# Kernel tuning notes

Measured on AMD Instinct MI355X. Metric: run time of the kernel, lower is better.

Reference implementation:

```python
import jax, jax.numpy as jnp
import numpy as np

TOP_K = 8


def setup_inputs() -> dict:
    key = jax.random.key(0)
    k1, k2, k3, k4, k5 = jax.random.split(key, 5)
    B, S, H, E, I = 1, 2048, 2048, 32, 768
    return {
        "hidden_states": jax.random.normal(k1, (B, S, H), dtype=jnp.float32),
        "gate_w": jax.random.normal(k2, (E, H), dtype=jnp.float32) * (H ** -0.5),
        "w_gate_proj": jax.random.normal(k3, (E, I, H), dtype=jnp.float32) * (H ** -0.5),
        "w_up_proj": jax.random.normal(k4, (E, I, H), dtype=jnp.float32) * (H ** -0.5),
        "w_down_proj": jax.random.normal(k5, (E, H, I), dtype=jnp.float32) * (I ** -0.5),
    }


def _masked_routing(router_logits):
    # norm_topk_prob=True branch: topk logits -> softmax over the k selected
    T, E = router_logits.shape
    sel_w, sel_e = jax.lax.top_k(router_logits, TOP_K)          # [T,k]
    sel_w = jax.nn.softmax(sel_w.astype(jnp.float32), axis=1)    # [T,k]
    rows = jnp.arange(T)[:, None]
    masked = jnp.zeros((T, E), dtype=jnp.float32).at[rows, sel_e].set(sel_w)
    count = jnp.zeros((E,), dtype=jnp.int32).at[sel_e.reshape(-1)].add(1)
    return masked, count


def reference(hidden_states, gate_w, w_gate_proj, w_up_proj, w_down_proj):
    B, S, H = hidden_states.shape
    x = hidden_states.reshape(-1, H)                              # [T,H]
    router_logits = x @ gate_w.T                                  # [T,E]
    masked_w, _count = _masked_routing(router_logits)
    # custom_moe_glu: per-expert GLU MLP, combined with masked routing weights
    g = jnp.einsum("th,eih->tei", x, w_gate_proj)                # [T,E,I]
    u = jnp.einsum("th,eih->tei", x, w_up_proj)                  # [T,E,I]
    h = jax.nn.silu(g) * u                                        # [T,E,I]
    h = h * masked_w[:, :, None]                                  # zero unselected experts
    out = jnp.einsum("tei,ehi->th", h, w_down_proj)              # [T,H]
    return out.reshape(B, S, H)
```

## Files before the change

kernel.cpp:

```cpp
#include <hip/hip_runtime.h>

#define T_TOK 2048
#define H_DIM 2048
#define E_NUM 32
#define I_DIM 768
#define TOPK 8

typedef __attribute__((ext_vector_type(8))) _Float16 f16x8;
typedef __attribute__((ext_vector_type(4))) _Float16 f16x4;
typedef __attribute__((ext_vector_type(4))) float f32x4;

__global__ __launch_bounds__(256) void cvt_x_kernel(const float* __restrict__ x,
                                                    _Float16* __restrict__ xh) {
    int i = blockIdx.x * 256 + threadIdx.x;
    f32x4 f = ((const f32x4*)x)[i];
    f16x4 h;
    h[0] = (_Float16)f[0]; h[1] = (_Float16)f[1];
    h[2] = (_Float16)f[2]; h[3] = (_Float16)f[3];
    ((f16x4*)xh)[i] = h;
}

__global__ __launch_bounds__(256) void router_kernel(const float* __restrict__ x,
                                                     const float* __restrict__ gw,
                                                     int* __restrict__ sel_e,
                                                     float* __restrict__ sel_w,
                                                     int* __restrict__ counts) {
    int t = blockIdx.x;
    int tid = threadIdx.x, lane = tid & 63, wave = tid >> 6;
    __shared__ float logits[E_NUM];
    const float* xr = x + (size_t)t * H_DIM;
    float xv[32];
#pragma unroll
    for (int c = 0; c < 32; ++c) xv[c] = xr[lane + c * 64];
    for (int j = 0; j < 8; ++j) {
        int e = wave * 8 + j;
        const float* wr = gw + (size_t)e * H_DIM;
        float acc = 0.f;
#pragma unroll
        for (int c = 0; c < 32; ++c) acc += xv[c] * wr[lane + c * 64];
#pragma unroll
        for (int s = 32; s > 0; s >>= 1) acc += __shfl_xor(acc, s, 64);
        if (lane == 0) logits[e] = acc;
    }
    __syncthreads();
    if (tid == 0) {
        float lg[E_NUM];
        for (int e2 = 0; e2 < E_NUM; ++e2) lg[e2] = logits[e2];
        unsigned taken = 0;
        float sv[TOPK]; int se[TOPK];
        for (int k = 0; k < TOPK; ++k) {
            float best = -3.4e38f; int bi = 0;
            for (int e2 = 0; e2 < E_NUM; ++e2)
                if (!((taken >> e2) & 1u) && lg[e2] > best) { best = lg[e2]; bi = e2; }
            taken |= 1u << bi; sv[k] = best; se[k] = bi;
        }
        float m = sv[0], s = 0.f;
        for (int k = 0; k < TOPK; ++k) { sv[k] = expf(sv[k] - m); s += sv[k]; }
        float inv = 1.f / s;
        for (int k = 0; k < TOPK; ++k) {
            sel_e[t * TOPK + k] = se[k];
            sel_w[t * TOPK + k] = sv[k] * inv;
            atomicAdd(&counts[se[k]], 1);
        }
    }
}

__global__ void scan_kernel(const int* __restrict__ counts, int* __restrict__ offs) {
    if (threadIdx.x == 0) {
        int s = 0;
        for (int e = 0; e < E_NUM; ++e) { offs[e] = s; s += counts[e]; }
        offs[E_NUM] = s;
    }
}

__global__ __launch_bounds__(256) void scatter_kernel(const int* __restrict__ sel_e,
                                                      const float* __restrict__ sel_w,
                                                      const int* __restrict__ offs,
                                                      int* __restrict__ cursor,
                                                      int* __restrict__ pair_token,
                                                      float* __restrict__ pair_w) {
    int t = blockIdx.x * 256 + threadIdx.x;
    if (t >= T_TOK) return;
    for (int k = 0; k < TOPK; ++k) {
        int e = sel_e[t * TOPK + k];
        int pos = atomicAdd(&cursor[e], 1);
        int slot = offs[e] + pos;
        pair_token[slot] = t;
        pair_w[slot] = sel_w[t * TOPK + k];
    }
}

__global__ __launch_bounds__(256, 2) void mlp1_kernel(const _Float16* __restrict__ xh,
                                                      const float* __restrict__ wg,
                                                      const float* __restrict__ wu,
                                                      const int* __restrict__ offs,
                                                      const int* __restrict__ pair_token,
                                                      const float* __restrict__ pair_w,
                                                      _Float16* __restrict__ h_buf) {
    int e = blockIdx.z, mt = blockIdx.y, nt = blockIdx.x;
    int base = offs[e], cnt = offs[e + 1] - base;
    if (mt * 128 >= cnt) return;
    int tid = threadIdx.x, lane = tid & 63, wave = tid >> 6;

    __shared__ _Float16 As[128 * 40];
    __shared__ _Float16 Bg[128 * 40];
    __shared__ _Float16 Bu[128 * 40];

    const _Float16* aSrc[2]; int aDst[2];
#pragma unroll
    for (int i = 0; i < 2; ++i) {
        int c = tid + i * 256;
        int row = c >> 2, col8 = c & 3;
        int g = mt * 128 + row;
        int tok = (g < cnt) ? pair_token[base + g] : pair_token[base];
        aSrc[i] = xh + (size_t)tok * H_DIM + col8 * 8;
        aDst[i] = row * 40 + col8 * 8;
    }
    const float* gSrc[4]; const float* uSrc[4]; int bDst[4];
#pragma unroll
    for (int i = 0; i < 4; ++i) {
        int c = tid + i * 256;
        int row = c >> 3, col4 = c & 7;
        size_t wOff = ((size_t)e * I_DIM + nt * 128 + row) * H_DIM + col4 * 4;
        gSrc[i] = wg + wOff; uSrc[i] = wu + wOff;
        bDst[i] = row * 40 + col4 * 4;
    }

    const f32x4 zero = {0.f, 0.f, 0.f, 0.f};
    f32x4 accg[4][4], accu[4][4];
#pragma unroll
    for (int mi = 0; mi < 4; ++mi)
#pragma unroll
        for (int ni = 0; ni < 4; ++ni) { accg[mi][ni] = zero; accu[mi][ni] = zero; }

    int m16 = lane & 15, quad = lane >> 4, wm = wave >> 1, wn = wave & 1;

    for (int k0 = 0; k0 < H_DIM; k0 += 32) {
#pragma unroll
        for (int i = 0; i < 2; ++i)
            *(f16x8*)&As[aDst[i]] = *(const f16x8*)(aSrc[i] + k0);
#pragma unroll
        for (int i = 0; i < 4; ++i) {
            f32x4 fg = *(const f32x4*)(gSrc[i] + k0);
            f32x4 fu = *(const f32x4*)(uSrc[i] + k0);
            f16x4 hg, hu;
#pragma unroll
            for (int q = 0; q < 4; ++q) { hg[q] = (_Float16)fg[q]; hu[q] = (_Float16)fu[q]; }
            *(f16x4*)&Bg[bDst[i]] = hg;
            *(f16x4*)&Bu[bDst[i]] = hu;
        }
        __syncthreads();
        f16x8 a[4], bg[4], bu[4];
#pragma unroll
        for (int mi = 0; mi < 4; ++mi)
            a[mi] = *(const f16x8*)&As[(wm * 64 + mi * 16 + m16) * 40 + quad * 8];
#pragma unroll
        for (int ni = 0; ni < 4; ++ni) {
            int r = (wn * 64 + ni * 16 + m16) * 40 + quad * 8;
            bg[ni] = *(const f16x8*)&Bg[r];
            bu[ni] = *(const f16x8*)&Bu[r];
        }
#pragma unroll
        for (int mi = 0; mi < 4; ++mi)
#pragma unroll
            for (int ni = 0; ni < 4; ++ni) {
                accg[mi][ni] = __builtin_amdgcn_mfma_f32_16x16x32_f16(a[mi], bg[ni], accg[mi][ni], 0, 0, 0);
                accu[mi][ni] = __builtin_amdgcn_mfma_f32_16x16x32_f16(a[mi], bu[ni], accu[mi][ni], 0, 0, 0);
            }
        __syncthreads();
    }

#pragma unroll
    for (int mi = 0; mi < 4; ++mi) {
#pragma unroll
        for (int reg = 0; reg < 4; ++reg) {
            int rloc = wm * 64 + mi * 16 + quad * 4 + reg;
            int g = mt * 128 + rloc;
            if (g >= cnt) continue;
            int slot = base + g;
            float pw = pair_w[slot];
#pragma unroll
            for (int ni = 0; ni < 4; ++ni) {
                int col = nt * 128 + wn * 64 + ni * 16 + m16;
                float gv = accg[mi][ni][reg];
                float uv = accu[mi][ni][reg];
                float hv = (gv / (1.f + expf(-gv))) * uv * pw;
                h_buf[(size_t)slot * I_DIM + col] = (_Float16)hv;
            }
        }
    }
}

__global__ __launch_bounds__(256, 2) void mlp2_kernel(const _Float16* __restrict__ h_buf,
                                                      const float* __restrict__ wd,
                                                      const int* __restrict__ offs,
                                                      const int* __restrict__ pair_token,
                                                      float* __restrict__ out) {
    int e = blockIdx.z, mt = blockIdx.y, nt = blockIdx.x;
    int base = offs[e], cnt = offs[e + 1] - base;
    if (mt * 128 >= cnt) return;
    int tid = threadIdx.x, lane = tid & 63, wave = tid >> 6;

    __shared__ _Float16 As[128 * 40];
    __shared__ _Float16 Bs[128 * 40];

    const _Float16* aSrc[2]; int aDst[2];
#pragma unroll
    for (int i = 0; i < 2; ++i) {
        int c = tid + i * 256;
        int row = c >> 2, col8 = c & 3;
        int g = mt * 128 + row;
        int slot = (g < cnt) ? (base + g) : base;
        aSrc[i] = h_buf + (size_t)slot * I_DIM + col8 * 8;
        aDst[i] = row * 40 + col8 * 8;
    }
    const float* bSrc[4]; int bDst[4];
#pragma unroll
    for (int i = 0; i < 4; ++i) {
        int c = tid + i * 256;
        int row = c >> 3, col4 = c & 7;
        bSrc[i] = wd + ((size_t)e * H_DIM + nt * 128 + row) * I_DIM + col4 * 4;
        bDst[i] = row * 40 + col4 * 4;
    }

    const f32x4 zero = {0.f, 0.f, 0.f, 0.f};
    f32x4 acc[4][4];
#pragma unroll
    for (int mi = 0; mi < 4; ++mi)
#pragma unroll
        for (int ni = 0; ni < 4; ++ni) acc[mi][ni] = zero;

    int m16 = lane & 15, quad = lane >> 4, wm = wave >> 1, wn = wave & 1;

    for (int k0 = 0; k0 < I_DIM; k0 += 32) {
#pragma unroll
        for (int i = 0; i < 2; ++i)
            *(f16x8*)&As[aDst[i]] = *(const f16x8*)(aSrc[i] + k0);
#pragma unroll
        for (int i = 0; i < 4; ++i) {
            f32x4 f = *(const f32x4*)(bSrc[i] + k0);
            f16x4 h;
#pragma unroll
            for (int q = 0; q < 4; ++q) h[q] = (_Float16)f[q];
            *(f16x4*)&Bs[bDst[i]] = h;
        }
        __syncthreads();
        f16x8 a[4], b[4];
#pragma unroll
        for (int mi = 0; mi < 4; ++mi)
            a[mi] = *(const f16x8*)&As[(wm * 64 + mi * 16 + m16) * 40 + quad * 8];
#pragma unroll
        for (int ni = 0; ni < 4; ++ni)
            b[ni] = *(const f16x8*)&Bs[(wn * 64 + ni * 16 + m16) * 40 + quad * 8];
#pragma unroll
        for (int mi = 0; mi < 4; ++mi)
#pragma unroll
            for (int ni = 0; ni < 4; ++ni)
                acc[mi][ni] = __builtin_amdgcn_mfma_f32_16x16x32_f16(a[mi], b[ni], acc[mi][ni], 0, 0, 0);
        __syncthreads();
    }

#pragma unroll
    for (int mi = 0; mi < 4; ++mi) {
#pragma unroll
        for (int reg = 0; reg < 4; ++reg) {
            int rloc = wm * 64 + mi * 16 + quad * 4 + reg;
            int g = mt * 128 + rloc;
            if (g >= cnt) continue;
            int t = pair_token[base + g];
#pragma unroll
            for (int ni = 0; ni < 4; ++ni) {
                int col = nt * 128 + wn * 64 + ni * 16 + m16;
                atomicAdd(&out[(size_t)t * H_DIM + col], acc[mi][ni][reg]);
            }
        }
    }
}

extern "C" void kernel_launch(void* const* d_in, const int* in_sizes, int n_in,
                              void* d_out, int out_size, void* d_ws, size_t ws_size,
                              hipStream_t stream) {
    const float* x  = (const float*)d_in[0];
    const float* gw = (const float*)d_in[1];
    const float* wg = (const float*)d_in[2];
    const float* wu = (const float*)d_in[3];
    const float* wd = (const float*)d_in[4];
    float* out = (float*)d_out;

    char* ws = (char*)d_ws;
    int*      sel_e      = (int*)(ws + 0);
    float*    sel_w      = (float*)(ws + 65536);
    int*      counts     = (int*)(ws + 131072);
    int*      cursor     = (int*)(ws + 131200);
    int*      offs       = (int*)(ws + 131328);
    int*      pair_token = (int*)(ws + 131584);
    float*    pair_w     = (float*)(ws + 197120);
    _Float16* xh         = (_Float16*)(ws + 262656);
    _Float16* h_buf      = (_Float16*)(ws + 8651264);

    hipMemsetAsync(ws + 131072, 0, 256, stream);
    hipMemsetAsync(d_out, 0, (size_t)T_TOK * H_DIM * sizeof(float), stream);

    cvt_x_kernel<<<(T_TOK * H_DIM / 4) / 256, 256, 0, stream>>>(x, xh);
    router_kernel<<<T_TOK, 256, 0, stream>>>(x, gw, sel_e, sel_w, counts);
    scan_kernel<<<1, 64, 0, stream>>>(counts, offs);
    scatter_kernel<<<T_TOK / 256, 256, 0, stream>>>(sel_e, sel_w, offs, cursor, pair_token, pair_w);
    mlp1_kernel<<<dim3(6, 16, 32), 256, 0, stream>>>(xh, wg, wu, offs, pair_token, pair_w, h_buf);
    mlp2_kernel<<<dim3(16, 16, 32), 256, 0, stream>>>(h_buf, wd, offs, pair_token, out);
}
```

Before: 954.0 us.

## Reshape MoE GEMM tiles to 256x64 and parallelize router top-k with wave shuffles

Changes both expert GEMM kernels from 128x128 tiles to 256-row by 64-column tiles, with each wave owning 64 rows. Fewer fp32 weight elements are loaded and converted per tile, so weight traffic per output is meant to drop as token rows increase. Grid order is swapped so row tiles vary fastest, which may improve L2 reuse of weight tiles across blocks. The router's serial single-thread top-k becomes a wave-wide shuffle argmax, with the tradeoff that experts averaging ~512 tokens leave partially empty 256-row tiles.

```diff
diff --git a/kernel.cpp b/kernel.cpp
--- a/kernel.cpp
+++ b/kernel.cpp
@@ -43,24 +43,33 @@
         if (lane == 0) logits[e] = acc;
     }
     __syncthreads();
-    if (tid == 0) {
-        float lg[E_NUM];
-        for (int e2 = 0; e2 < E_NUM; ++e2) lg[e2] = logits[e2];
-        unsigned taken = 0;
+    if (wave == 0) {
+        float v = (lane < E_NUM) ? logits[lane] : -3.4e38f;
+        int idx = lane;
         float sv[TOPK]; int se[TOPK];
+#pragma unroll
         for (int k = 0; k < TOPK; ++k) {
-            float best = -3.4e38f; int bi = 0;
-            for (int e2 = 0; e2 < E_NUM; ++e2)
-                if (!((taken >> e2) & 1u) && lg[e2] > best) { best = lg[e2]; bi = e2; }
-            taken |= 1u << bi; sv[k] = best; se[k] = bi;
-        }
-        float m = sv[0], s = 0.f;
-        for (int k = 0; k < TOPK; ++k) { sv[k] = expf(sv[k] - m); s += sv[k]; }
-        float inv = 1.f / s;
-        for (int k = 0; k < TOPK; ++k) {
-            sel_e[t * TOPK + k] = se[k];
-            sel_w[t * TOPK + k] = sv[k] * inv;
-            atomicAdd(&counts[se[k]], 1);
+            float bv = v; int bi = idx;
+#pragma unroll
+            for (int s = 32; s > 0; s >>= 1) {
+                float ov = __shfl_xor(bv, s, 64);
+                int oi = __shfl_xor(bi, s, 64);
+                if (ov > bv || (ov == bv && oi < bi)) { bv = ov; bi = oi; }
+            }
+            sv[k] = bv; se[k] = bi;
+            if (lane == bi) v = -3.4e38f;
+        }
+        if (lane == 0) {
+            float m = sv[0], s = 0.f;
+#pragma unroll
+            for (int k = 0; k < TOPK; ++k) { sv[k] = expf(sv[k] - m); s += sv[k]; }
+            float inv = 1.f / s;
+#pragma unroll
+            for (int k = 0; k < TOPK; ++k) {
+                sel_e[t * TOPK + k] = se[k];
+                sel_w[t * TOPK + k] = sv[k] * inv;
+                atomicAdd(&counts[se[k]], 1);
+            }
         }
     }
 }
@@ -97,31 +106,31 @@
                                                       const int* __restrict__ pair_token,
                                                       const float* __restrict__ pair_w,
                                                       _Float16* __restrict__ h_buf) {
-    int e = blockIdx.z, mt = blockIdx.y, nt = blockIdx.x;
+    int mt = blockIdx.x, nt = blockIdx.y, e = blockIdx.z;
     int base = offs[e], cnt = offs[e + 1] - base;
-    if (mt * 128 >= cnt) return;
+    if (mt * 256 >= cnt) return;
     int tid = threadIdx.x, lane = tid & 63, wave = tid >> 6;
 
-    __shared__ _Float16 As[128 * 40];
-    __shared__ _Float16 Bg[128 * 40];
-    __shared__ _Float16 Bu[128 * 40];
-
-    const _Float16* aSrc[2]; int aDst[2];
-#pragma unroll
-    for (int i = 0; i < 2; ++i) {
+    __shared__ _Float16 As[256 * 40];
+    __shared__ _Float16 Bg[64 * 40];
+    __shared__ _Float16 Bu[64 * 40];
+
+    const _Float16* aSrc[4]; int aDst[4];
+#pragma unroll
+    for (int i = 0; i < 4; ++i) {
         int c = tid + i * 256;
         int row = c >> 2, col8 = c & 3;
-        int g = mt * 128 + row;
+        int g = mt * 256 + row;
         int tok = (g < cnt) ? pair_token[base + g] : pair_token[base];
         aSrc[i] = xh + (size_t)tok * H_DIM + col8 * 8;
         aDst[i] = row * 40 + col8 * 8;
     }
-    const float* gSrc[4]; const float* uSrc[4]; int bDst[4];
-#pragma unroll
-    for (int i = 0; i < 4; ++i) {
+    const float* gSrc[2]; const float* uSrc[2]; int bDst[2];
+#pragma unroll
+    for (int i = 0; i < 2; ++i) {
         int c = tid + i * 256;
         int row = c >> 3, col4 = c & 7;
-        size_t wOff = ((size_t)e * I_DIM + nt * 128 + row) * H_DIM + col4 * 4;
+        size_t wOff = ((size_t)e * I_DIM + nt * 64 + row) * H_DIM + col4 * 4;
         gSrc[i] = wg + wOff; uSrc[i] = wu + wOff;
         bDst[i] = row * 40 + col4 * 4;
     }
@@ -133,14 +142,14 @@
 #pragma unroll
         for (int ni = 0; ni < 4; ++ni) { accg[mi][ni] = zero; accu[mi][ni] = zero; }
 
-    int m16 = lane & 15, quad = lane >> 4, wm = wave >> 1, wn = wave & 1;
+    int m16 = lane & 15, quad = lane >> 4, wm = wave;
 
     for (int k0 = 0; k0 < H_DIM; k0 += 32) {
 #pragma unroll
-        for (int i = 0; i < 2; ++i)
+        for (int i = 0; i < 4; ++i)
             *(f16x8*)&As[aDst[i]] = *(const f16x8*)(aSrc[i] + k0);
 #pragma unroll
-        for (int i = 0; i < 4; ++i) {
+        for (int i = 0; i < 2; ++i) {
             f32x4 fg = *(const f32x4*)(gSrc[i] + k0);
             f32x4 fu = *(const f32x4*)(uSrc[i] + k0);
             f16x4 hg, hu;
@@ -156,7 +165,7 @@
             a[mi] = *(const f16x8*)&As[(wm * 64 + mi * 16 + m16) * 40 + quad * 8];
 #pragma unroll
         for (int ni = 0; ni < 4; ++ni) {
-            int r = (wn * 64 + ni * 16 + m16) * 40 + quad * 8;
+            int r = (ni * 16 + m16) * 40 + quad * 8;
             bg[ni] = *(const f16x8*)&Bg[r];
             bu[ni] = *(const f16x8*)&Bu[r];
         }
@@ -175,13 +184,13 @@
 #pragma unroll
         for (int reg = 0; reg < 4; ++reg) {
             int rloc = wm * 64 + mi * 16 + quad * 4 + reg;
-            int g = mt * 128 + rloc;
+            int g = mt * 256 + rloc;
             if (g >= cnt) continue;
             int slot = base + g;
             float pw = pair_w[slot];
 #pragma unroll
             for (int ni = 0; ni < 4; ++ni) {
-                int col = nt * 128 + wn * 64 + ni * 16 + m16;
+                int col = nt * 64 + ni * 16 + m16;
                 float gv = accg[mi][ni][reg];
                 float uv = accu[mi][ni][reg];
                 float hv = (gv / (1.f + expf(-gv))) * uv * pw;
@@ -196,30 +205,30 @@
                                                       const int* __restrict__ offs,
                                                       const int* __restrict__ pair_token,
                                                       float* __restrict__ out) {
-    int e = blockIdx.z, mt = blockIdx.y, nt = blockIdx.x;
+    int mt = blockIdx.x, nt = blockIdx.y, e = blockIdx.z;
     int base = offs[e], cnt = offs[e + 1] - base;
-    if (mt * 128 >= cnt) return;
+    if (mt * 256 >= cnt) return;
     int tid = threadIdx.x, lane = tid & 63, wave = tid >> 6;
 
-    __shared__ _Float16 As[128 * 40];
-    __shared__ _Float16 Bs[128 * 40];
-
-    const _Float16* aSrc[2]; int aDst[2];
-#pragma unroll
-    for (int i = 0; i < 2; ++i) {
+    __shared__ _Float16 As[256 * 40];
+    __shared__ _Float16 Bs[64 * 40];
+
+    const _Float16* aSrc[4]; int aDst[4];
+#pragma unroll
+    for (int i = 0; i < 4; ++i) {
         int c = tid + i * 256;
         int row = c >> 2, col8 = c & 3;
-        int g = mt * 128 + row;
+        int g = mt * 256 + row;
         int slot = (g < cnt) ? (base + g) : base;
         aSrc[i] = h_buf + (size_t)slot * I_DIM + col8 * 8;
         aDst[i] = row * 40 + col8 * 8;
     }
-    const float* bSrc[4]; int bDst[4];
-#pragma unroll
-    for (int i = 0; i < 4; ++i) {
+    const float* bSrc[2]; int bDst[2];
+#pragma unroll
+    for (int i = 0; i < 2; ++i) {
         int c = tid + i * 256;
         int row = c >> 3, col4 = c & 7;
-        bSrc[i] = wd + ((size_t)e * H_DIM + nt * 128 + row) * I_DIM + col4 * 4;
+        bSrc[i] = wd + ((size_t)e * H_DIM + nt * 64 + row) * I_DIM + col4 * 4;
         bDst[i] = row * 40 + col4 * 4;
     }
 
@@ -230,14 +239,14 @@
 #pragma unroll
         for (int ni = 0; ni < 4; ++ni) acc[mi][ni] = zero;
 
-    int m16 = lane & 15, quad = lane >> 4, wm = wave >> 1, wn = wave & 1;
+    int m16 = lane & 15, quad = lane >> 4, wm = wave;
 
     for (int k0 = 0; k0 < I_DIM; k0 += 32) {
 #pragma unroll
-        for (int i = 0; i < 2; ++i)
+        for (int i = 0; i < 4; ++i)
             *(f16x8*)&As[aDst[i]] = *(const f16x8*)(aSrc[i] + k0);
 #pragma unroll
-        for (int i = 0; i < 4; ++i) {
+        for (int i = 0; i < 2; ++i) {
             f32x4 f = *(const f32x4*)(bSrc[i] + k0);
             f16x4 h;
 #pragma unroll
@@ -251,7 +260,7 @@
             a[mi] = *(const f16x8*)&As[(wm * 64 + mi * 16 + m16) * 40 + quad * 8];
 #pragma unroll
         for (int ni = 0; ni < 4; ++ni)
-            b[ni] = *(const f16x8*)&Bs[(wn * 64 + ni * 16 + m16) * 40 + quad * 8];
+            b[ni] = *(const f16x8*)&Bs[(ni * 16 + m16) * 40 + quad * 8];
 #pragma unroll
         for (int mi = 0; mi < 4; ++mi)
 #pragma unroll
@@ -265,12 +274,12 @@
 #pragma unroll
         for (int reg = 0; reg < 4; ++reg) {
             int rloc = wm * 64 + mi * 16 + quad * 4 + reg;
-            int g = mt * 128 + rloc;
+            int g = mt * 256 + rloc;
             if (g >= cnt) continue;
             int t = pair_token[base + g];
 #pragma unroll
             for (int ni = 0; ni < 4; ++ni) {
-                int col = nt * 128 + wn * 64 + ni * 16 + m16;
+                int col = nt * 64 + ni * 16 + m16;
                 atomicAdd(&out[(size_t)t * H_DIM + col], acc[mi][ni][reg]);
             }
         }
@@ -305,6 +314,6 @@
     router_kernel<<<T_TOK, 256, 0, stream>>>(x, gw, sel_e, sel_w, counts);
     scan_kernel<<<1, 64, 0, stream>>>(counts, offs);
     scatter_kernel<<<T_TOK / 256, 256, 0, stream>>>(sel_e, sel_w, offs, cursor, pair_token, pair_w);
-    mlp1_kernel<<<dim3(6, 16, 32), 256, 0, stream>>>(xh, wg, wu, offs, pair_token, pair_w, h_buf);
-    mlp2_kernel<<<dim3(16, 16, 32), 256, 0, stream>>>(h_buf, wd, offs, pair_token, out);
-}
+    mlp1_kernel<<<dim3(8, 12, 32), 256, 0, stream>>>(xh, wg, wu, offs, pair_token, pair_w, h_buf);
+    mlp2_kernel<<<dim3(8, 32, 32), 256, 0, stream>>>(h_buf, wd, offs, pair_token, out);
+}
```

Result: slower. 1.600 ms (+67.7%).
